# Optimization experiments

Hardware: AMD Instinct MI355X
Metric: run time of the kernel (lower is better)

Reference implementation:

```python
import jax, jax.numpy as jnp
import numpy as np

DECAY = 0.99
EPS = 1e-05
COMMIT = 0.25


def setup_inputs() -> dict:
    key = jax.random.key(0)
    k1, k2 = jax.random.split(key)
    dim, n_embed = 256, 8192
    z = jax.random.normal(k1, (32, 32, 32, dim), dtype=jnp.float32)
    embed = jax.random.normal(k2, (dim, n_embed), dtype=jnp.float32)
    cluster_size = jnp.zeros((n_embed,), dtype=jnp.float32)
    embed_avg = embed  # torch init: embed_avg = embed.clone()
    return {"z": z, "embed": embed, "cluster_size": cluster_size, "embed_avg": embed_avg}


def reference(z, embed, cluster_size, embed_avg):
    dim, n_embed = embed.shape
    flatten = z.reshape(-1, dim)                       # [N, D]
    # squared L2 distance to each code: ||f||^2 - 2 f.E + ||E||^2
    dist = ((flatten ** 2).sum(1, keepdims=True)
            - 2.0 * flatten @ embed
            + (embed ** 2).sum(0, keepdims=True))      # [N, K]
    ind = jnp.argmin(dist, axis=1)                     # [N]
    quantize = jnp.take(embed.T, ind, axis=0).reshape(z.shape)
    embed_ind = ind.reshape(z.shape[:-1])

    # EMA codebook update (training mode), via segment_sum instead of a dense one-hot
    counts = jax.ops.segment_sum(jnp.ones_like(ind, dtype=flatten.dtype), ind,
                                 num_segments=n_embed)          # [K]
    embed_sum = jax.ops.segment_sum(flatten, ind,
                                    num_segments=n_embed).T     # [D, K]
    cluster_size_new = cluster_size * DECAY + (1.0 - DECAY) * counts
    embed_avg_new = embed_avg * DECAY + (1.0 - DECAY) * embed_sum
    n = cluster_size_new.sum()
    cs = (cluster_size_new + EPS) / (n + n_embed * EPS) * n
    embed_new = embed_avg_new / cs[None, :]

    diff = COMMIT * jnp.mean((jax.lax.stop_gradient(quantize) - z) ** 2)
    quantize_st = z + jax.lax.stop_gradient(quantize - z)  # straight-through
    return quantize_st, diff, embed_ind, embed_new
```

## Files before the change

### kernel.cpp

```cpp
#include <hip/hip_runtime.h>
#include <hip/hip_bf16.h>

#define D 256
#define K 8192
#define NTOT 32768
#define BM 128
#define BN2 128
#define BD 32
#define CSPLIT 4
#define CT_PER (K / CSPLIT / BN2)

typedef __bf16 bf16x8 __attribute__((ext_vector_type(8)));
typedef float f32x4 __attribute__((ext_vector_type(4)));

__device__ __forceinline__ void gl_lds16(const void* g, void* l) {
    __builtin_amdgcn_global_load_lds(
        (__attribute__((address_space(1))) void*)(g),
        (__attribute__((address_space(3))) void*)(l), 16, 0, 0);
}

__device__ __forceinline__ unsigned int enc_f32(float f) {
    unsigned int u = __float_as_uint(f);
    return (u & 0x80000000u) ? ~u : (u | 0x80000000u);
}

__device__ __forceinline__ unsigned short f2bfu(float x) {
    __hip_bfloat16 h = __float2bfloat16(x);
    return __builtin_bit_cast(unsigned short, h);
}
__device__ __forceinline__ float bfu2f(unsigned short u) {
    return __bfloat162float(__builtin_bit_cast(__hip_bfloat16, u));
}

__global__ __launch_bounds__(256)
void conv_F(const float* __restrict__ z, unsigned short* __restrict__ Fhi,
            unsigned short* __restrict__ Flo) {
    int i4 = blockIdx.x * 256 + threadIdx.x;
    float4 v = ((const float4*)z)[i4];
    ushort4 h, l;
    h.x = f2bfu(v.x); l.x = f2bfu(v.x - bfu2f(h.x));
    h.y = f2bfu(v.y); l.y = f2bfu(v.y - bfu2f(h.y));
    h.z = f2bfu(v.z); l.z = f2bfu(v.z - bfu2f(h.z));
    h.w = f2bfu(v.w); l.w = f2bfu(v.w - bfu2f(h.w));
    ((ushort4*)Fhi)[i4] = h;
    ((ushort4*)Flo)[i4] = l;
}

__global__ __launch_bounds__(256)
void conv_E(const float* __restrict__ E, unsigned short* __restrict__ EhiT,
            unsigned short* __restrict__ EloT, float* __restrict__ ET,
            float* __restrict__ enorm) {
    __shared__ float tile[64][65];
    int tid = threadIdx.x;
    int k0 = blockIdx.x * 64, d0 = blockIdx.y * 64;
#pragma unroll
    for (int it = 0; it < 16; ++it) {
        int idx = it * 256 + tid;
        int dr = idx >> 6, kc = idx & 63;
        tile[kc][dr] = E[(d0 + dr) * K + k0 + kc];
    }
    __syncthreads();
#pragma unroll
    for (int it = 0; it < 16; ++it) {
        int idx = it * 256 + tid;
        int kr = idx >> 6, dc = idx & 63;
        float v = tile[kr][dc];
        unsigned short h = f2bfu(v);
        int o = (k0 + kr) * D + d0 + dc;
        EhiT[o] = h;
        EloT[o] = f2bfu(v - bfu2f(h));
        ET[o] = v;
        float p = v * v;
#pragma unroll
        for (int off = 32; off; off >>= 1) p += __shfl_down(p, off);
        if ((tid & 63) == 0) atomicAdd(&enorm[k0 + kr], p);
    }
}

__global__ __launch_bounds__(256)
void mfma_dist_argmin(const unsigned short* __restrict__ Fhi,
                      const unsigned short* __restrict__ Flo,
                      const unsigned short* __restrict__ EhiT,
                      const unsigned short* __restrict__ EloT,
                      const float* __restrict__ enorm,
                      unsigned long long* __restrict__ bestpack) {
    __shared__ unsigned short Ah[BM * BD], Al[BM * BD], Bh[BN2 * BD], Bl[BN2 * BD];

    const int tid = threadIdx.x;
    const int wave = tid >> 6;
    const int lane = tid & 63;
    const int qd = lane >> 4;
    const int ln = lane & 15;
    const int wm = (wave >> 1) * 64;
    const int wn = (wave & 1) * 64;
    const int n0 = blockIdx.x * BM;
    const int c0 = blockIdx.y * (K / CSPLIT);
    const int r_ = tid >> 2;
    const int s_sw = (tid & 3) ^ ((tid >> 3) & 3);
    const int csw = (qd ^ ((ln >> 1) & 3)) * 8;

    int aro[4], bro[4];
#pragma unroll
    for (int mi = 0; mi < 4; ++mi) aro[mi] = (wm + mi * 16 + ln) * BD + csw;
#pragma unroll
    for (int ni = 0; ni < 4; ++ni) bro[ni] = (wn + ni * 16 + ln) * BD + csw;

    float bestv[16];
    int besti[16];
#pragma unroll
    for (int i = 0; i < 16; ++i) { bestv[i] = 3.402823466e38f; besti[i] = 0; }

    for (int ct = 0; ct < CT_PER; ++ct) {
        const int cb = c0 + ct * BN2;
        f32x4 acc[4][4];
#pragma unroll
        for (int mi = 0; mi < 4; ++mi)
#pragma unroll
            for (int ni = 0; ni < 4; ++ni) acc[mi][ni] = (f32x4){0.f, 0.f, 0.f, 0.f};

        for (int d0 = 0; d0 < D; d0 += BD) {
            __syncthreads();
#pragma unroll
            for (int it = 0; it < 2; ++it) {
                const int ga = (n0 + it * 64 + r_) * D + d0 + s_sw * 8;
                const int gb = (cb + it * 64 + r_) * D + d0 + s_sw * 8;
                const int lo = it * 2048 + wave * 512;
                gl_lds16(Fhi + ga, &Ah[lo]);
                gl_lds16(Flo + ga, &Al[lo]);
                gl_lds16(EhiT + gb, &Bh[lo]);
                gl_lds16(EloT + gb, &Bl[lo]);
            }
            __syncthreads();

            bf16x8 a0[4], b0[4], b1[4];
#pragma unroll
            for (int mi = 0; mi < 4; ++mi) a0[mi] = *(const bf16x8*)&Ah[aro[mi]];
#pragma unroll
            for (int ni = 0; ni < 4; ++ni) b0[ni] = *(const bf16x8*)&Bh[bro[ni]];
#pragma unroll
            for (int mi = 0; mi < 4; ++mi)
#pragma unroll
                for (int ni = 0; ni < 4; ++ni)
                    acc[mi][ni] = __builtin_amdgcn_mfma_f32_16x16x32_bf16(
                        a0[mi], b0[ni], acc[mi][ni], 0, 0, 0);
#pragma unroll
            for (int ni = 0; ni < 4; ++ni) b1[ni] = *(const bf16x8*)&Bl[bro[ni]];
#pragma unroll
            for (int mi = 0; mi < 4; ++mi)
#pragma unroll
                for (int ni = 0; ni < 4; ++ni)
                    acc[mi][ni] = __builtin_amdgcn_mfma_f32_16x16x32_bf16(
                        a0[mi], b1[ni], acc[mi][ni], 0, 0, 0);
#pragma unroll
            for (int mi = 0; mi < 4; ++mi) a0[mi] = *(const bf16x8*)&Al[aro[mi]];
#pragma unroll
            for (int mi = 0; mi < 4; ++mi)
#pragma unroll
                for (int ni = 0; ni < 4; ++ni)
                    acc[mi][ni] = __builtin_amdgcn_mfma_f32_16x16x32_bf16(
                        a0[mi], b0[ni], acc[mi][ni], 0, 0, 0);
        }

#pragma unroll
        for (int ni = 0; ni < 4; ++ni) {
            int k = cb + wn + ni * 16 + ln;
            float en = enorm[k];
#pragma unroll
            for (int mi = 0; mi < 4; ++mi) {
                f32x4 a = acc[mi][ni];
#pragma unroll
                for (int r = 0; r < 4; ++r) {
                    float dist = en - 2.0f * a[r];
                    int bi = mi * 4 + r;
                    if (dist < bestv[bi]) { bestv[bi] = dist; besti[bi] = k; }
                }
            }
        }
    }

#pragma unroll
    for (int mi = 0; mi < 4; ++mi) {
#pragma unroll
        for (int r = 0; r < 4; ++r) {
            int bi = mi * 4 + r;
            float v = bestv[bi];
            int ix = besti[bi];
#pragma unroll
            for (int off = 1; off < 16; off <<= 1) {
                float v2 = __shfl_xor(v, off);
                int i2 = __shfl_xor(ix, off);
                if (v2 < v || (v2 == v && i2 < ix)) { v = v2; ix = i2; }
            }
            if (ln == 0) {
                int m = n0 + wm + mi * 16 + qd * 4 + r;
                unsigned long long pack =
                    ((unsigned long long)enc_f32(v) << 32) | (unsigned int)ix;
                atomicMin(&bestpack[m], pack);
            }
        }
    }
}

#define ROWS_PER_BLOCK 16
__global__ __launch_bounds__(256)
void assign_apply(const float* __restrict__ z,
                  const float* __restrict__ ET,
                  const unsigned long long* __restrict__ bestpack,
                  float* __restrict__ out_q, float* __restrict__ out_ind,
                  float* __restrict__ out_diff,
                  float* __restrict__ counts, float* __restrict__ esumT) {
    const int tx = threadIdx.x;
    const int rbase = blockIdx.x * ROWS_PER_BLOCK;
    float part = 0.f;
#pragma unroll 4
    for (int r = 0; r < ROWS_PER_BLOCK; ++r) {
        int n = rbase + r;
        unsigned long long p = bestpack[n];
        int idx = (int)(p & 0xFFFFFFFFull);
        float f = z[n * D + tx];
        float q = ET[idx * D + tx];
        out_q[n * D + tx] = q;
        float dd = q - f;
        part += dd * dd;
        atomicAdd(&esumT[idx * D + tx], f);
        if (tx == 0) {
            atomicAdd(&counts[idx], 1.0f);
            out_ind[n] = (float)idx;
        }
    }
#pragma unroll
    for (int off = 32; off; off >>= 1) part += __shfl_down(part, off);
    __shared__ float wsum[4];
    if ((tx & 63) == 0) wsum[tx >> 6] = part;
    __syncthreads();
    if (tx == 0) {
        float t = wsum[0] + wsum[1] + wsum[2] + wsum[3];
        atomicAdd(out_diff, t * (0.25f / 8388608.0f));
    }
}

__global__ __launch_bounds__(1024)
void csn_sum(const float* __restrict__ cs_in, const float* __restrict__ counts,
             float* __restrict__ csn, float* __restrict__ nsum) {
    const float decay = 0.99f;
    const float omd = 0.01f;
    int k = blockIdx.x * 1024 + threadIdx.x;
    float v = decay * cs_in[k] + omd * counts[k];
    csn[k] = v;
    float p = v;
#pragma unroll
    for (int off = 32; off; off >>= 1) p += __shfl_down(p, off);
    __shared__ float red[16];
    if ((threadIdx.x & 63) == 0) red[threadIdx.x >> 6] = p;
    __syncthreads();
    if (threadIdx.x == 0) {
        float t = 0.f;
#pragma unroll
        for (int i = 0; i < 16; ++i) t += red[i];
        atomicAdd(nsum, t);
    }
}

__global__ __launch_bounds__(256)
void finalize(const float* __restrict__ eavg, const float* __restrict__ esumT,
              const float* __restrict__ csn, const float* __restrict__ nsum,
              float* __restrict__ out_enew) {
    const float decay = 0.99f;
    const float omd = 0.01f;
    const float keps = (float)(8192 * 1e-5);
    int idx = blockIdx.x * 256 + threadIdx.x;
    float nv = nsum[0];
    int k = idx & (K - 1);
    int d = idx >> 13;
    float avg_new = decay * eavg[idx] + omd * esumT[k * D + d];
    float cs = (csn[k] + 1e-5f) / (nv + keps) * nv;
    out_enew[idx] = avg_new / cs;
}

extern "C" void kernel_launch(void* const* d_in, const int* in_sizes, int n_in,
                              void* d_out, int out_size, void* d_ws, size_t ws_size,
                              hipStream_t stream) {
    const float* z = (const float*)d_in[0];
    const float* embed = (const float*)d_in[1];
    const float* cs_in = (const float*)d_in[2];
    const float* eavg = (const float*)d_in[3];

    float* out = (float*)d_out;
    float* out_q = out;
    float* out_diff = out + 8388608;
    float* out_ind = out + 8388609;
    float* out_enew = out + 8421377;

    char* ws = (char*)d_ws;
    unsigned long long* bestpack = (unsigned long long*)ws;
    float* enorm = (float*)(ws + 262144);
    float* counts = (float*)(ws + 294912);
    float* csn = (float*)(ws + 327680);
    float* nsum = (float*)(ws + 360448);
    float* esumT = (float*)(ws + 360704);
    unsigned short* Fhi = (unsigned short*)(ws + 8749312);
    unsigned short* Flo = (unsigned short*)(ws + 25526528);
    unsigned short* EhiT = (unsigned short*)(ws + 42303744);
    unsigned short* EloT = (unsigned short*)(ws + 46498048);
    float* ET = (float*)(ws + 50692352);

    hipMemsetAsync(bestpack, 0xFF, NTOT * 8, stream);
    hipMemsetAsync(ws + 262144, 0, 8749312 - 262144, stream);
    hipMemsetAsync(out_diff, 0, 4, stream);

    conv_F<<<NTOT * D / 4 / 256, 256, 0, stream>>>(z, Fhi, Flo);
    conv_E<<<dim3(K / 64, D / 64), 256, 0, stream>>>(embed, EhiT, EloT, ET, enorm);
    mfma_dist_argmin<<<dim3(NTOT / BM, CSPLIT), 256, 0, stream>>>(Fhi, Flo, EhiT, EloT,
                                                                  enorm, bestpack);
    assign_apply<<<NTOT / ROWS_PER_BLOCK, 256, 0, stream>>>(z, ET, bestpack, out_q,
                                                            out_ind, out_diff, counts, esumT);
    csn_sum<<<K / 1024, 1024, 0, stream>>>(cs_in, counts, csn, nsum);
    finalize<<<(D * K) / 256, 256, 0, stream>>>(eavg, esumT, csn, nsum, out_enew);
}
```

Measured before the change: 600.0 us.

## Halve distance-kernel row tile to 64 and merge conversion kernels into one launch

The distance/argmin GEMM tile shrinks from 128 to 64 rows per block, so each wave holds 2x4 MFMA accumulators instead of 4x4. This doubles the grid and cuts register use, which should raise occupancy, at the cost of loading each codebook tile twice as often. The two input-conversion kernels are also fused into a single launch that picks its branch by block index, removing one kernel launch.

```diff
diff --git a/kernel.cpp b/kernel.cpp
--- a/kernel.cpp
+++ b/kernel.cpp
@@ -4,7 +4,7 @@
 #define D 256
 #define K 8192
 #define NTOT 32768
-#define BM 128
+#define BM 64
 #define BN2 128
 #define BD 32
 #define CSPLIT 4
@@ -32,27 +32,29 @@
     return __bfloat162float(__builtin_bit_cast(__hip_bfloat16, u));
 }
 
+#define CONVF_BLOCKS (NTOT * D / 4 / 256)
 __global__ __launch_bounds__(256)
-void conv_F(const float* __restrict__ z, unsigned short* __restrict__ Fhi,
-            unsigned short* __restrict__ Flo) {
-    int i4 = blockIdx.x * 256 + threadIdx.x;
-    float4 v = ((const float4*)z)[i4];
-    ushort4 h, l;
-    h.x = f2bfu(v.x); l.x = f2bfu(v.x - bfu2f(h.x));
-    h.y = f2bfu(v.y); l.y = f2bfu(v.y - bfu2f(h.y));
-    h.z = f2bfu(v.z); l.z = f2bfu(v.z - bfu2f(h.z));
-    h.w = f2bfu(v.w); l.w = f2bfu(v.w - bfu2f(h.w));
-    ((ushort4*)Fhi)[i4] = h;
-    ((ushort4*)Flo)[i4] = l;
-}
-
-__global__ __launch_bounds__(256)
-void conv_E(const float* __restrict__ E, unsigned short* __restrict__ EhiT,
-            unsigned short* __restrict__ EloT, float* __restrict__ ET,
-            float* __restrict__ enorm) {
+void conv_all(const float* __restrict__ z, unsigned short* __restrict__ Fhi,
+              unsigned short* __restrict__ Flo, const float* __restrict__ E,
+              unsigned short* __restrict__ EhiT, unsigned short* __restrict__ EloT,
+              float* __restrict__ ET, float* __restrict__ enorm) {
+    int bx = blockIdx.x;
+    int tid = threadIdx.x;
+    if (bx < CONVF_BLOCKS) {
+        int i4 = bx * 256 + tid;
+        float4 v = ((const float4*)z)[i4];
+        ushort4 h, l;
+        h.x = f2bfu(v.x); l.x = f2bfu(v.x - bfu2f(h.x));
+        h.y = f2bfu(v.y); l.y = f2bfu(v.y - bfu2f(h.y));
+        h.z = f2bfu(v.z); l.z = f2bfu(v.z - bfu2f(h.z));
+        h.w = f2bfu(v.w); l.w = f2bfu(v.w - bfu2f(h.w));
+        ((ushort4*)Fhi)[i4] = h;
+        ((ushort4*)Flo)[i4] = l;
+        return;
+    }
     __shared__ float tile[64][65];
-    int tid = threadIdx.x;
-    int k0 = blockIdx.x * 64, d0 = blockIdx.y * 64;
+    int idx2 = bx - CONVF_BLOCKS;
+    int k0 = (idx2 & 127) * 64, d0 = (idx2 >> 7) * 64;
 #pragma unroll
     for (int it = 0; it < 16; ++it) {
         int idx = it * 256 + tid;
@@ -84,14 +86,15 @@
                       const unsigned short* __restrict__ EloT,
                       const float* __restrict__ enorm,
                       unsigned long long* __restrict__ bestpack) {
-    __shared__ unsigned short Ah[BM * BD], Al[BM * BD], Bh[BN2 * BD], Bl[BN2 * BD];
+    __shared__ unsigned short Ah[BM * BD], Al[BM * BD];
+    __shared__ unsigned short Bh[BN2 * BD], Bl[BN2 * BD];
 
     const int tid = threadIdx.x;
     const int wave = tid >> 6;
     const int lane = tid & 63;
     const int qd = lane >> 4;
     const int ln = lane & 15;
-    const int wm = (wave >> 1) * 64;
+    const int wm = (wave >> 1) * 32;
     const int wn = (wave & 1) * 64;
     const int n0 = blockIdx.x * BM;
     const int c0 = blockIdx.y * (K / CSPLIT);
@@ -99,46 +102,49 @@
     const int s_sw = (tid & 3) ^ ((tid >> 3) & 3);
     const int csw = (qd ^ ((ln >> 1) & 3)) * 8;
 
-    int aro[4], bro[4];
-#pragma unroll
-    for (int mi = 0; mi < 4; ++mi) aro[mi] = (wm + mi * 16 + ln) * BD + csw;
+    int aro[2], bro[4];
+#pragma unroll
+    for (int mi = 0; mi < 2; ++mi) aro[mi] = (wm + mi * 16 + ln) * BD + csw;
 #pragma unroll
     for (int ni = 0; ni < 4; ++ni) bro[ni] = (wn + ni * 16 + ln) * BD + csw;
 
-    float bestv[16];
-    int besti[16];
-#pragma unroll
-    for (int i = 0; i < 16; ++i) { bestv[i] = 3.402823466e38f; besti[i] = 0; }
+    float bestv[8];
+    int besti[8];
+#pragma unroll
+    for (int i = 0; i < 8; ++i) { bestv[i] = 3.402823466e38f; besti[i] = 0; }
 
     for (int ct = 0; ct < CT_PER; ++ct) {
         const int cb = c0 + ct * BN2;
-        f32x4 acc[4][4];
-#pragma unroll
-        for (int mi = 0; mi < 4; ++mi)
+        f32x4 acc[2][4];
+#pragma unroll
+        for (int mi = 0; mi < 2; ++mi)
 #pragma unroll
             for (int ni = 0; ni < 4; ++ni) acc[mi][ni] = (f32x4){0.f, 0.f, 0.f, 0.f};
 
         for (int d0 = 0; d0 < D; d0 += BD) {
             __syncthreads();
+            {
+                const int ga = (n0 + r_) * D + d0 + s_sw * 8;
+                const int lo = wave * 512;
+                gl_lds16(Fhi + ga, &Ah[lo]);
+                gl_lds16(Flo + ga, &Al[lo]);
+            }
 #pragma unroll
             for (int it = 0; it < 2; ++it) {
-                const int ga = (n0 + it * 64 + r_) * D + d0 + s_sw * 8;
                 const int gb = (cb + it * 64 + r_) * D + d0 + s_sw * 8;
                 const int lo = it * 2048 + wave * 512;
-                gl_lds16(Fhi + ga, &Ah[lo]);
-                gl_lds16(Flo + ga, &Al[lo]);
                 gl_lds16(EhiT + gb, &Bh[lo]);
                 gl_lds16(EloT + gb, &Bl[lo]);
             }
             __syncthreads();
 
-            bf16x8 a0[4], b0[4], b1[4];
-#pragma unroll
-            for (int mi = 0; mi < 4; ++mi) a0[mi] = *(const bf16x8*)&Ah[aro[mi]];
+            bf16x8 a0[2], b0[4], b1[4];
+#pragma unroll
+            for (int mi = 0; mi < 2; ++mi) a0[mi] = *(const bf16x8*)&Ah[aro[mi]];
 #pragma unroll
             for (int ni = 0; ni < 4; ++ni) b0[ni] = *(const bf16x8*)&Bh[bro[ni]];
 #pragma unroll
-            for (int mi = 0; mi < 4; ++mi)
+            for (int mi = 0; mi < 2; ++mi)
 #pragma unroll
                 for (int ni = 0; ni < 4; ++ni)
                     acc[mi][ni] = __builtin_amdgcn_mfma_f32_16x16x32_bf16(
@@ -146,15 +152,15 @@
 #pragma unroll
             for (int ni = 0; ni < 4; ++ni) b1[ni] = *(const bf16x8*)&Bl[bro[ni]];
 #pragma unroll
-            for (int mi = 0; mi < 4; ++mi)
+            for (int mi = 0; mi < 2; ++mi)
 #pragma unroll
                 for (int ni = 0; ni < 4; ++ni)
                     acc[mi][ni] = __builtin_amdgcn_mfma_f32_16x16x32_bf16(
                         a0[mi], b1[ni], acc[mi][ni], 0, 0, 0);
 #pragma unroll
-            for (int mi = 0; mi < 4; ++mi) a0[mi] = *(const bf16x8*)&Al[aro[mi]];
-#pragma unroll
-            for (int mi = 0; mi < 4; ++mi)
+            for (int mi = 0; mi < 2; ++mi) a0[mi] = *(const bf16x8*)&Al[aro[mi]];
+#pragma unroll
+            for (int mi = 0; mi < 2; ++mi)
 #pragma unroll
                 for (int ni = 0; ni < 4; ++ni)
                     acc[mi][ni] = __builtin_amdgcn_mfma_f32_16x16x32_bf16(
@@ -166,7 +172,7 @@
             int k = cb + wn + ni * 16 + ln;
             float en = enorm[k];
 #pragma unroll
-            for (int mi = 0; mi < 4; ++mi) {
+            for (int mi = 0; mi < 2; ++mi) {
                 f32x4 a = acc[mi][ni];
 #pragma unroll
                 for (int r = 0; r < 4; ++r) {
@@ -179,7 +185,7 @@
     }
 
 #pragma unroll
-    for (int mi = 0; mi < 4; ++mi) {
+    for (int mi = 0; mi < 2; ++mi) {
 #pragma unroll
         for (int r = 0; r < 4; ++r) {
             int bi = mi * 4 + r;
@@ -308,8 +314,8 @@
     hipMemsetAsync(ws + 262144, 0, 8749312 - 262144, stream);
     hipMemsetAsync(out_diff, 0, 4, stream);
 
-    conv_F<<<NTOT * D / 4 / 256, 256, 0, stream>>>(z, Fhi, Flo);
-    conv_E<<<dim3(K / 64, D / 64), 256, 0, stream>>>(embed, EhiT, EloT, ET, enorm);
+    conv_all<<<CONVF_BLOCKS + 512, 256, 0, stream>>>(z, Fhi, Flo, embed, EhiT, EloT,
+                                                     ET, enorm);
     mfma_dist_argmin<<<dim3(NTOT / BM, CSPLIT), 256, 0, stream>>>(Fhi, Flo, EhiT, EloT,
                                                                   enorm, bestpack);
     assign_apply<<<NTOT / ROWS_PER_BLOCK, 256, 0, stream>>>(z, ET, bestpack, out_q,
```

Measured after the change: 669.6 us. +11.6%, slower.
